# Optimization experiments

Hardware: AMD Instinct MI355X
Metric: run time of the kernel (lower is better)

The kernel has to match this reference:

```python
import jax, jax.numpy as jnp
import numpy as np

BEV_X = 128
BEV_Y = 128
NUM_VOXELS = BEV_X * BEV_Y


def setup_inputs() -> dict:
    key = jax.random.key(0)
    k1, k2, k3 = jax.random.split(key, 3)
    B, N, D, H, W, C = 2, 6, 112, 16, 44, 80
    depth_logits = jax.random.normal(k1, (B, N, D, H, W), dtype=jnp.float32)
    context = jax.random.normal(k2, (B, N, C, H, W), dtype=jnp.float32)
    geom_idx = jax.random.randint(k3, (B, N, D, H, W), 0, NUM_VOXELS, dtype=jnp.int32)
    return {"depth_logits": depth_logits, "context": context, "geom_idx": geom_idx}


def reference(depth_logits, context, geom_idx):
    # depth_logits: [B,N,D,H,W], context: [B,N,C,H,W], geom_idx: [B,N,D,H,W] in [0, NUM_VOXELS)
    B, N, D, H, W = depth_logits.shape
    C = context.shape[2]
    # softmax over depth bins -> per-pixel depth distribution
    depth = jax.nn.softmax(depth_logits, axis=2)
    # lift: outer product depth x context -> [B,N,D,H,W,C]
    feat = jnp.einsum('bndhw,bnchw->bndhwc', depth, context)
    P = N * D * H * W
    feat = feat.reshape(B * P, C)
    # splat: scatter-add each frustum point into its BEV voxel (batch-offset indices)
    idx = (geom_idx.reshape(B, P) + jnp.arange(B, dtype=jnp.int32)[:, None] * NUM_VOXELS).reshape(-1)
    bev = jax.ops.segment_sum(feat, idx, num_segments=B * NUM_VOXELS)
    # [B, C, BEV_Y, BEV_X]
    return bev.reshape(B, BEV_Y, BEV_X, C).transpose(0, 3, 1, 2)
```

## Files before the change

kernel.cpp:

```cpp
#include <hip/hip_runtime.h>
#include <hip/hip_bf16.h>


constexpr int B = 2, N = 6, D = 112, H = 16, W = 44, C = 80;
constexpr int HW = H * W;
constexpr int NPIX = B * N * HW;
constexpr int NV = 128 * 128;
constexpr int PTS = NPIX * D;
constexpr int DHW = D * HW;
constexpr int NBKT = 512;
constexpr int CAP = 2816;

__global__ __launch_bounds__(NBKT) void init_cursor_kernel(
    int* __restrict__ cursor) {
  cursor[threadIdx.x] = threadIdx.x * CAP;
}

__global__ __launch_bounds__(256) void fused_scatter_kernel(
    const float* __restrict__ logits, const float* __restrict__ ctx,
    const int* __restrict__ gidx, float* __restrict__ ctxT,
    int* __restrict__ cursor, uint2* __restrict__ sorted) {
  const int t = threadIdx.x;
  const int pix0 = blockIdx.x * 64;
  const int bn = pix0 / HW;
  const int hw0 = pix0 - bn * HW;
  const int b = bn / N;

  __shared__ float tile[C][65];
  __shared__ float redm[4][64], reds[4][64];
  __shared__ int hist[NBKT], sbase[NBKT];

  const float* src = ctx + (size_t)bn * C * HW + hw0;
#pragma unroll
  for (int it = 0; it < (C * 64) / 256; ++it) {
    const int idx = it * 256 + t;
    const int c = idx >> 6;
    const int i = idx & 63;
    tile[c][i] = src[(size_t)c * HW + i];
  }
  hist[t] = 0;
  hist[t + 256] = 0;
  __syncthreads();
  {
    float* dst = ctxT + (size_t)pix0 * C;
#pragma unroll
    for (int it = 0; it < (C * 64) / 256; ++it) {
      const int j = it * 256 + t;
      const int pl = j / C;
      const int c = j - pl * C;
      dst[j] = tile[c][pl];
    }
  }

  const int l = t & 63;
  const int q = t >> 6;
  const int hw = hw0 + l;
  const int pix = pix0 + l;
  const int d0 = q * 28;
  const float* lg = logits + (size_t)bn * DHW + hw;

  float x[28];
  float m = -3.0e38f;
#pragma unroll
  for (int j = 0; j < 28; ++j) {
    x[j] = lg[(size_t)(d0 + j) * HW];
    m = fmaxf(m, x[j]);
  }
  redm[q][l] = m;
  __syncthreads();
  m = fmaxf(fmaxf(redm[0][l], redm[1][l]), fmaxf(redm[2][l], redm[3][l]));
  float s = 0.0f;
#pragma unroll
  for (int j = 0; j < 28; ++j) {
    x[j] = __expf(x[j] - m);
    s += x[j];
  }
  reds[q][l] = s;
  __syncthreads();
  const float inv =
      1.0f / (reds[0][l] + reds[1][l] + reds[2][l] + reds[3][l]);

  const int* gi = gidx + (size_t)bn * DHW + hw;
  unsigned w0[28];
  int rank[28];
#pragma unroll
  for (int j = 0; j < 28; ++j) {
    const int fb = b * NV + gi[(size_t)(d0 + j) * HW];
    w0[j] = (unsigned)pix | ((unsigned)fb << 16);
    x[j] *= inv;
    rank[j] = atomicAdd(&hist[w0[j] >> 22], 1);
  }
  __syncthreads();

  for (int k = t; k < NBKT; k += 256) {
    const int c_ = hist[k];
    sbase[k] = c_ ? atomicAdd(&cursor[k], c_) : 0;
  }
  __syncthreads();

#pragma unroll
  for (int j = 0; j < 28; ++j) {
    const int bk = w0[j] >> 22;
    const int pos = sbase[bk] + rank[j];
    if (pos < (bk + 1) * CAP)
      sorted[pos] = make_uint2(w0[j], __float_as_uint(x[j]));
  }
}

__global__ __launch_bounds__(512) void bucket_gather_kernel(
    const float* __restrict__ ctxT, const uint2* __restrict__ sorted,
    const int* __restrict__ cursor, float* __restrict__ out) {
  const int t = threadIdx.x;
  const int g = blockIdx.x;
  const int b = g >> 8;
  const int vox0 = (g & 255) * 64;

  __shared__ uint2 srec[CAP];
  __shared__ float tile[64][80];
  __shared__ int shist[64], soff[64];

  if (t < 64) shist[t] = 0;
  __syncthreads();

  int cnt = cursor[g] - g * CAP;
  if (cnt > CAP) cnt = CAP;
  const uint2* rec = sorted + (size_t)g * CAP;

  uint2 rr[6];
  int rk[6];
#pragma unroll
  for (int k = 0; k < 6; ++k) {
    const int idx = t + k * 512;
    rk[k] = -1;
    if (idx < cnt) {
      rr[k] = rec[idx];
      rk[k] = atomicAdd(&shist[(rr[k].x >> 16) & 63], 1);
    }
  }
  __syncthreads();

  if (t < 64) {
    const int v = shist[t];
    int xx = v;
#pragma unroll
    for (int o = 1; o < 64; o <<= 1) {
      const int y = __shfl_up(xx, o, 64);
      if (t >= o) xx += y;
    }
    soff[t] = xx - v;
  }
  __syncthreads();

#pragma unroll
  for (int k = 0; k < 6; ++k) {
    if (rk[k] >= 0) {
      const int v = (rr[k].x >> 16) & 63;
      srec[soff[v] + rk[k]] = rr[k];
    }
  }
  __syncthreads();

  const int w = t >> 6;
  const int l = t & 63;
  for (int j = 0; j < 8; ++j) {
    const int v = w * 8 + j;
    const int s0 = soff[v];
    const int n = shist[v];
    float a0 = 0.0f, a1 = 0.0f;
    int k = 0;
    for (; k + 4 <= n; k += 4) {
      const uint2 ra = srec[s0 + k + 0];
      const uint2 rb = srec[s0 + k + 1];
      const uint2 rc = srec[s0 + k + 2];
      const uint2 rd = srec[s0 + k + 3];
      const float* wa = ctxT + (size_t)(ra.x & 0xFFFFu) * C;
      const float* wb = ctxT + (size_t)(rb.x & 0xFFFFu) * C;
      const float* wc = ctxT + (size_t)(rc.x & 0xFFFFu) * C;
      const float* wd = ctxT + (size_t)(rd.x & 0xFFFFu) * C;
      const float pa = __uint_as_float(ra.y);
      const float pb = __uint_as_float(rb.y);
      const float pc = __uint_as_float(rc.y);
      const float pd = __uint_as_float(rd.y);
      a0 += pa * wa[l];
      a0 += pb * wb[l];
      a0 += pc * wc[l];
      a0 += pd * wd[l];
      if (l < 16) {
        a1 += pa * wa[64 + l];
        a1 += pb * wb[64 + l];
        a1 += pc * wc[64 + l];
        a1 += pd * wd[64 + l];
      }
    }
    for (; k < n; ++k) {
      const uint2 ra = srec[s0 + k];
      const float* wa = ctxT + (size_t)(ra.x & 0xFFFFu) * C;
      const float pa = __uint_as_float(ra.y);
      a0 += pa * wa[l];
      if (l < 16) a1 += pa * wa[64 + l];
    }
    tile[v][l] = a0;
    if (l < 16) tile[v][64 + l] = a1;
  }
  __syncthreads();

  const size_t ob = (size_t)b * C * NV + vox0;
#pragma unroll
  for (int i = 0; i < 10; ++i) {
    const int idx = i * 512 + t;
    const int c = idx >> 6;
    const int v = idx & 63;
    out[ob + (size_t)c * NV + v] = tile[v][c];
  }
}

__global__ __launch_bounds__(256) void lift_splat_direct_kernel(
    const float* __restrict__ logits, const float* __restrict__ ctx,
    const int* __restrict__ gidx, float* __restrict__ out) {
  const int t = threadIdx.x;
  const int pix = blockIdx.x;
  const int hw = pix % HW;
  const int bn = pix / HW;
  const int b = bn / N;

  const float* lg = logits + (size_t)bn * DHW + hw;
  const int* gi = gidx + (size_t)bn * DHW + hw;
  const float* cx = ctx + (size_t)bn * (C * HW) + hw;

  __shared__ float s_prob[D];
  __shared__ float s_ctx[C];
  __shared__ int s_idx[D];
  __shared__ float red[256];

  float v = -3.0e38f;
  if (t < D) {
    v = lg[(size_t)t * HW];
    s_idx[t] = gi[(size_t)t * HW];
  }
  if (t < C) s_ctx[t] = cx[(size_t)t * HW];

  red[t] = v;
  __syncthreads();
#pragma unroll
  for (int s = 128; s >= 1; s >>= 1) {
    if (t < s) red[t] = fmaxf(red[t], red[t + s]);
    __syncthreads();
  }
  const float m = red[0];
  __syncthreads();

  const float e = (t < D) ? __expf(v - m) : 0.0f;
  red[t] = e;
  __syncthreads();
#pragma unroll
  for (int s = 128; s >= 1; s >>= 1) {
    if (t < s) red[t] += red[t + s];
    __syncthreads();
  }
  const float inv = 1.0f / red[0];
  if (t < D) s_prob[t] = e * inv;
  __syncthreads();

  for (int f = t; f < D * C; f += 256) {
    const int d = f / C;
    const int c = f - d * C;
    atomicAdd(&out[((size_t)(b * C + c)) * NV + s_idx[d]],
              s_prob[d] * s_ctx[c]);
  }
}

extern "C" void kernel_launch(void* const* d_in, const int* in_sizes, int n_in,
                              void* d_out, int out_size, void* d_ws,
                              size_t ws_size, hipStream_t stream) {
  const float* logits = (const float*)d_in[0];
  const float* ctx = (const float*)d_in[1];
  const int* gidx = (const int*)d_in[2];
  float* out = (float*)d_out;

  size_t off = 0;
  uint2* sorted = (uint2*)((char*)d_ws + off);
  off += (size_t)NBKT * CAP * sizeof(uint2);
  float* ctxT = (float*)((char*)d_ws + off);
  off += (size_t)NPIX * C * sizeof(float);
  int* cursor = (int*)((char*)d_ws + off);
  off += (size_t)NBKT * sizeof(int);

  if (ws_size >= off) {
    init_cursor_kernel<<<1, NBKT, 0, stream>>>(cursor);
    fused_scatter_kernel<<<NPIX / 64, 256, 0, stream>>>(logits, ctx, gidx,
                                                        ctxT, cursor, sorted);
    bucket_gather_kernel<<<NBKT, 512, 0, stream>>>(ctxT, sorted, cursor, out);
  } else {
    (void)hipMemsetAsync(d_out, 0, (size_t)out_size * sizeof(float), stream);
    lift_splat_direct_kernel<<<NPIX, 256, 0, stream>>>(logits, ctx, gidx, out);
  }
}
```

Baseline: 113.4 us.

## Split fused softmax/scatter into prep and per-batch bucket scatter kernels

Splits the fused kernel in two. One kernel computes the depth softmax, writes probabilities to a workspace buffer and transposes context. A second kernel, with smaller 16-pixel blocks, reads the probabilities and indices and bucket-scatters records into the sorted buffer. The scatter uses 256 buckets per batch, which shrinks the per-block histogram and raises block count and parallelism. In exchange it adds a full round trip of the probability tensor through global memory and one more kernel launch.

```diff
diff --git a/kernel.cpp b/kernel.cpp
--- a/kernel.cpp
+++ b/kernel.cpp
@@ -16,19 +16,16 @@
   cursor[threadIdx.x] = threadIdx.x * CAP;
 }
 
-__global__ __launch_bounds__(256) void fused_scatter_kernel(
+__global__ __launch_bounds__(256) void prep_kernel(
     const float* __restrict__ logits, const float* __restrict__ ctx,
-    const int* __restrict__ gidx, float* __restrict__ ctxT,
-    int* __restrict__ cursor, uint2* __restrict__ sorted) {
+    float* __restrict__ probD, float* __restrict__ ctxT) {
   const int t = threadIdx.x;
   const int pix0 = blockIdx.x * 64;
   const int bn = pix0 / HW;
   const int hw0 = pix0 - bn * HW;
-  const int b = bn / N;
 
   __shared__ float tile[C][65];
   __shared__ float redm[4][64], reds[4][64];
-  __shared__ int hist[NBKT], sbase[NBKT];
 
   const float* src = ctx + (size_t)bn * C * HW + hw0;
 #pragma unroll
@@ -38,8 +35,6 @@
     const int i = idx & 63;
     tile[c][i] = src[(size_t)c * HW + i];
   }
-  hist[t] = 0;
-  hist[t + 256] = 0;
   __syncthreads();
   {
     float* dst = ctxT + (size_t)pix0 * C;
@@ -55,7 +50,6 @@
   const int l = t & 63;
   const int q = t >> 6;
   const int hw = hw0 + l;
-  const int pix = pix0 + l;
   const int d0 = q * 28;
   const float* lg = logits + (size_t)bn * DHW + hw;
 
@@ -80,30 +74,55 @@
   const float inv =
       1.0f / (reds[0][l] + reds[1][l] + reds[2][l] + reds[3][l]);
 
-  const int* gi = gidx + (size_t)bn * DHW + hw;
-  unsigned w0[28];
-  int rank[28];
-#pragma unroll
-  for (int j = 0; j < 28; ++j) {
-    const int fb = b * NV + gi[(size_t)(d0 + j) * HW];
-    w0[j] = (unsigned)pix | ((unsigned)fb << 16);
-    x[j] *= inv;
-    rank[j] = atomicAdd(&hist[w0[j] >> 22], 1);
-  }
-  __syncthreads();
-
-  for (int k = t; k < NBKT; k += 256) {
-    const int c_ = hist[k];
-    sbase[k] = c_ ? atomicAdd(&cursor[k], c_) : 0;
-  }
-  __syncthreads();
-
-#pragma unroll
-  for (int j = 0; j < 28; ++j) {
-    const int bk = w0[j] >> 22;
-    const int pos = sbase[bk] + rank[j];
-    if (pos < (bk + 1) * CAP)
-      sorted[pos] = make_uint2(w0[j], __float_as_uint(x[j]));
+  float* pd = probD + (size_t)bn * DHW + hw;
+#pragma unroll
+  for (int j = 0; j < 28; ++j) pd[(size_t)(d0 + j) * HW] = x[j] * inv;
+}
+
+__global__ __launch_bounds__(256) void bucket_scatter_kernel(
+    const float* __restrict__ probD, const int* __restrict__ gidx,
+    int* __restrict__ cursor, uint2* __restrict__ sorted) {
+  const int t = threadIdx.x;
+  const int blk = blockIdx.x;
+  const int bn = blk / 44;
+  const int hw0 = (blk - bn * 44) * 16;
+  const int b = bn / N;
+  const int pix0 = bn * HW + hw0;
+
+  __shared__ int hist[256], sbase[256];
+  hist[t] = 0;
+  __syncthreads();
+
+  const int l = t & 15;
+  const int q = t >> 4;
+  const size_t base = (size_t)bn * DHW + hw0 + l;
+
+  unsigned w0[7];
+  int rank[7];
+  float pv[7];
+#pragma unroll
+  for (int j = 0; j < 7; ++j) {
+    const int d = q * 7 + j;
+    const int fb = b * NV + gidx[base + (size_t)d * HW];
+    pv[j] = probD[base + (size_t)d * HW];
+    w0[j] = (unsigned)(pix0 + l) | ((unsigned)fb << 16);
+    rank[j] = atomicAdd(&hist[(w0[j] >> 22) & 255], 1);
+  }
+  __syncthreads();
+
+  {
+    const int c_ = hist[t];
+    sbase[t] = c_ ? atomicAdd(&cursor[(b << 8) | t], c_) : 0;
+  }
+  __syncthreads();
+
+#pragma unroll
+  for (int j = 0; j < 7; ++j) {
+    const int gb = w0[j] >> 22;
+    const int lb = gb & 255;
+    const int pos = sbase[lb] + rank[j];
+    if (pos < (gb + 1) * CAP)
+      sorted[pos] = make_uint2(w0[j], __float_as_uint(pv[j]));
   }
 }
 
@@ -280,6 +299,8 @@
   size_t off = 0;
   uint2* sorted = (uint2*)((char*)d_ws + off);
   off += (size_t)NBKT * CAP * sizeof(uint2);
+  float* probD = (float*)((char*)d_ws + off);
+  off += (size_t)PTS * sizeof(float);
   float* ctxT = (float*)((char*)d_ws + off);
   off += (size_t)NPIX * C * sizeof(float);
   int* cursor = (int*)((char*)d_ws + off);
@@ -287,8 +308,9 @@
 
   if (ws_size >= off) {
     init_cursor_kernel<<<1, NBKT, 0, stream>>>(cursor);
-    fused_scatter_kernel<<<NPIX / 64, 256, 0, stream>>>(logits, ctx, gidx,
-                                                        ctxT, cursor, sorted);
+    prep_kernel<<<NPIX / 64, 256, 0, stream>>>(logits, ctx, probD, ctxT);
+    bucket_scatter_kernel<<<B * N * (HW / 16), 256, 0, stream>>>(
+        probD, gidx, cursor, sorted);
     bucket_gather_kernel<<<NBKT, 512, 0, stream>>>(ctxT, sorted, cursor, out);
   } else {
     (void)hipMemsetAsync(d_out, 0, (size_t)out_size * sizeof(float), stream);
```

After: 114.0 us. No clear change (+0.6%).
